# Performance work log

Hardware: AMD Instinct MI355X
Metric: run time of the kernel (lower is better)

## Reference

```python
import jax, jax.numpy as jnp
import numpy as np

SEG_LENS = (2048, 4096, 8192)
DIL_RATES = (1, 2, 4)
DIM = 1024
HEADS = 16
HEAD_DIM = DIM // HEADS
BATCH = 1
SEQ = sum(SEG_LENS)


def _hilbert_perm(L):
    """Permutation ordering the first L row-major cells of a 2^k x 2^k grid by Hilbert distance."""
    n = 1
    while n * n < L:
        n *= 2
    idx = np.arange(n * n, dtype=np.int64)
    x = idx % n
    y = idx // n
    d = np.zeros(n * n, dtype=np.int64)
    s = n // 2
    while s > 0:
        rx = ((x & s) > 0).astype(np.int64)
        ry = ((y & s) > 0).astype(np.int64)
        d += s * s * ((3 * rx) ^ ry)
        swap = ry == 0
        flip = swap & (rx == 1)
        x = np.where(flip, s - 1 - x, x)
        y = np.where(flip, s - 1 - y, y)
        x, y = np.where(swap, y, x), np.where(swap, x, y)
        s //= 2
    return np.argsort(d[:L], kind='stable')


def _segment_attn(x_seg, wqkv, bqkv, wo, bo, rate, use_hilbert=True):
    """HilbertAttentionCore: hilbert reorder -> QKV -> dilated attention -> out proj -> inverse reorder.
    x_seg: [B, L, D] -> [B, L, D]
    """
    B, L, D = x_seg.shape
    hd = D // HEADS
    perm_np = _hilbert_perm(L)
    perm = jnp.asarray(perm_np)
    inv = jnp.asarray(np.argsort(perm_np))
    xh = x_seg[:, perm] if use_hilbert else x_seg
    qkv = xh @ wqkv + bqkv                      # [B, L, 3D]
    q, k, v = jnp.split(qkv, 3, axis=-1)
    q = q.reshape(B, L, HEADS, hd)
    k = k.reshape(B, L, HEADS, hd)
    v = v.reshape(B, L, HEADS, hd)
    Lr = L // rate
    offs = jnp.arange(HEADS) % rate             # per-head dilation offset
    hidx = jnp.arange(HEADS)

    def dilate(t):
        # position i = off + rate*j  <->  reshape(L//rate, rate)[j, off]
        tr = t.reshape(B, Lr, rate, HEADS, hd)
        return tr[:, :, offs, hidx, :]          # [B, Lr, H, hd]

    qd, kd, vd = dilate(q), dilate(k), dilate(v)
    scale = 1.0 / np.sqrt(hd).astype(np.float32)
    scores = jnp.einsum('bihd,bjhd->bhij', qd, kd) * scale
    probs = jax.nn.softmax(scores, axis=-1)
    od = jnp.einsum('bhij,bjhd->bihd', probs, vd)  # [B, Lr, H, hd]
    # scatter each head's dilated subsequence back; uncovered (head,pos) stay zero
    outr = jnp.zeros((B, Lr, rate, HEADS, hd), x_seg.dtype)
    outr = outr.at[:, :, offs, hidx, :].set(od)
    out = outr.reshape(B, L, HEADS * hd) @ wo + bo
    return out[:, inv] if use_hilbert else out


def setup_inputs() -> dict:
    key = jax.random.key(0)
    ks = jax.random.split(key, 16)
    inp = {
        'q': jax.random.normal(ks[0], (BATCH, SEQ, HEADS, HEAD_DIM), jnp.float32),
        'k': jax.random.normal(ks[1], (BATCH, SEQ, HEADS, HEAD_DIM), jnp.float32),
        'v': jax.random.normal(ks[2], (BATCH, SEQ, HEADS, HEAD_DIM), jnp.float32),
    }
    for i in range(3):
        inp[f'wqkv_{i}'] = jax.random.normal(ks[3 + 4 * i], (DIM, 3 * DIM), jnp.float32) * 0.02
        inp[f'bqkv_{i}'] = jnp.zeros((3 * DIM,), jnp.float32)
        inp[f'wo_{i}'] = jax.random.normal(ks[4 + 4 * i], (DIM, DIM), jnp.float32) * 0.02
        inp[f'bo_{i}'] = jnp.zeros((DIM,), jnp.float32)
    return inp


def reference(q, k, v,
              wqkv_0, bqkv_0, wo_0, bo_0,
              wqkv_1, bqkv_1, wo_1, bo_1,
              wqkv_2, bqkv_2, wo_2, bo_2):
    B, S, H, hd = q.shape
    x = q.reshape(B, S, H * hd)  # single-GPU path uses q only (as in the source)
    params = [(wqkv_0, bqkv_0, wo_0, bo_0),
              (wqkv_1, bqkv_1, wo_1, bo_1),
              (wqkv_2, bqkv_2, wo_2, bo_2)]
    outs = []
    pos = 0
    for (seg_len, rate), (wq, bq, wo, bo) in zip(zip(SEG_LENS, DIL_RATES), params):
        if pos >= S:
            break
        end = min(pos + seg_len, S)
        outs.append(_segment_attn(x[:, pos:end], wq, bq, wo, bo, rate))
        pos = end
    return jnp.concatenate(outs, axis=1).reshape(B, S, H, hd)
```

## Files before the change

kernel.cpp:

```cpp
#include <hip/hip_runtime.h>
#include <stdint.h>
#include <stddef.h>

typedef unsigned short u16;
typedef short bf16x8 __attribute__((ext_vector_type(8)));
typedef float f32x4 __attribute__((ext_vector_type(4)));
typedef float f32x16 __attribute__((ext_vector_type(16)));
typedef unsigned short ushort8v __attribute__((ext_vector_type(8)));
typedef int i32x2 __attribute__((ext_vector_type(2)));

#define LR 2048
#define LOG2E 1.44269504088896f

__device__ __forceinline__ u16 f2bf(float f) {
  unsigned u = __float_as_uint(f);
  unsigned r = u + 0x7fffu + ((u >> 16) & 1u);
  return (u16)(r >> 16);
}

__device__ __forceinline__ unsigned cvtpk(float lo, float hi) {
  unsigned r;
  asm("v_cvt_pk_bf16_f32 %0, %1, %2" : "=v"(r) : "v"(lo), "v"(hi));
  return r;
}

__device__ __forceinline__ void plswap(unsigned& a, unsigned& b) {
#if __has_builtin(__builtin_amdgcn_permlane32_swap)
  i32x2 r = __builtin_amdgcn_permlane32_swap((int)a, (int)b, false, false);
  a = (unsigned)r[0];
  b = (unsigned)r[1];
#else
  asm volatile("s_nop 1\n\tv_permlane32_swap_b32 %0, %1\n\ts_nop 1"
               : "+v"(a), "+v"(b));
#endif
}
__device__ __forceinline__ float xhalf_sum(float x) {
  unsigned a = __float_as_uint(x), b = __float_as_uint(x);
  plswap(a, b);
  return __uint_as_float(a) + __uint_as_float(b);
}

__device__ __forceinline__ void gl_lds16(const void* g, void* l) {
  __builtin_amdgcn_global_load_lds((__attribute__((address_space(1))) void*)g,
                                   (__attribute__((address_space(3))) void*)l,
                                   16, 0, 0);
}

__device__ __forceinline__ int hilbert_perm(int idx) {
  int seg = (idx < 2048) ? 0 : (idx < 6144 ? 1 : 2);
  int segpos = (seg == 0) ? 0 : (seg == 1 ? 2048 : 6144);
  int L = 2048 << seg;
  int n = (seg == 2) ? 128 : 64;
  int t = idx - segpos;
  int d = (L == n * n) ? t : ((t < (L >> 1)) ? t : t + L);
  int x = 0, y = 0;
  for (int s = 1; s < n; s <<= 1) {
    int rx = 1 & (d >> 1);
    int ry = 1 & (d ^ rx);
    if (ry == 0) {
      if (rx == 1) { x = s - 1 - x; y = s - 1 - y; }
      int tmp = x; x = y; y = tmp;
    }
    x += s * rx; y += s * ry;
    d >>= 2;
  }
  return y * n + x;
}

__global__ void wtrans_kernel(const float* __restrict__ q0, const float* __restrict__ q1,
                              const float* __restrict__ q2, const float* __restrict__ o0,
                              const float* __restrict__ o1, const float* __restrict__ o2,
                              u16* __restrict__ dq, u16* __restrict__ dw) {
  const int seg = blockIdx.z;
  const int bx = blockIdx.x;
  const int K = 1024;
  int tx = threadIdx.x, ty = threadIdx.y;
  __shared__ float tl[32][33];
  const float* S;
  u16* D;
  int N, n0, do_remap;
  if (bx < 96) {
    S = (seg == 0) ? q0 : (seg == 1 ? q1 : q2);
    D = dq + (size_t)seg * K * 3072;
    N = 3072; n0 = bx * 32; do_remap = 0;
  } else {
    S = (seg == 0) ? o0 : (seg == 1 ? o1 : o2);
    D = dw + (size_t)seg * K * 1024;
    N = 1024; n0 = (bx - 96) * 32; do_remap = 1;
  }
  int k0 = blockIdx.y * 32;
  #pragma unroll
  for (int i = 0; i < 4; i++)
    tl[ty + 8 * i][tx] = S[(size_t)(k0 + ty + 8 * i) * N + n0 + tx];
  __syncthreads();
  int kk = k0 + tx;
  if (do_remap) {
    int rate = 1 << seg;
    int h = kk >> 6;
    int h2 = (h & (rate - 1)) * (16 >> seg) + (h >> seg);
    kk = h2 * 64 + (kk & 63);
  }
  #pragma unroll
  for (int i = 0; i < 4; i++)
    D[(size_t)(n0 + ty + 8 * i) * K + kk] = f2bf(tl[tx][ty + 8 * i]);
}

__global__ void gather_kernel(const float* __restrict__ x, u16* __restrict__ xh) {
  int rr = blockIdx.x;
  int seg = (rr < 2048) ? 0 : (rr < 6144 ? 1 : 2);
  int segpos = (seg == 0) ? 0 : (seg == 1 ? 2048 : 6144);
  int rate = 1 << seg;
  int rl = rr - segpos;
  int t = (rl & (LR - 1)) * rate + (rl >> 11);
  int orig = segpos + hilbert_perm(segpos + t);
  float4 v = *((const float4*)(x + (size_t)orig * 1024) + threadIdx.x);
  ushort4 o;
  o.x = f2bf(v.x); o.y = f2bf(v.y); o.z = f2bf(v.z); o.w = f2bf(v.w);
  *((ushort4*)(xh + (size_t)rr * 1024) + threadIdx.x) = o;
}

__global__ __launch_bounds__(512, 2) void qkv_gemm_kernel(
    const u16* __restrict__ A, const u16* __restrict__ Bt,
    const float* __restrict__ b0, const float* __restrict__ b1,
    const float* __restrict__ b2, u16* __restrict__ C) {
  __shared__ char smem[131072];
  const int tid = threadIdx.x;
  const int lane = tid & 63, wid = tid >> 6;
  const int wm = wid >> 2, wn = wid & 3;
  const int bid = blockIdx.x;
  const int xcd = bid & 7;
  const int idx = bid >> 3;
  const int grp = idx / 42;
  const int rem = idx % 42;
  const int rb = xcd * 7 + rem / 6;
  const int nb = grp * 6 + rem % 6;
  const int seg = (rb < 8) ? 0 : (rb < 24 ? 1 : 2);
  const float* bias = (seg == 0) ? b0 : (seg == 1 ? b1 : b2);
  const size_t arow0 = (size_t)rb * 256;
  const char* Ab = (const char*)(A + arow0 * 1024);
  const char* Bb = (const char*)(Bt + ((size_t)seg * 3072 + (size_t)nb * 256) * 1024);

  f32x4 acc[8][4] = {};

  #pragma unroll
  for (int it = 0; it < 4; it++) {
    int p = (it * 512 + tid) * 16;
    int e = p ^ (((p >> 7) & 7) << 4);
    int row = e >> 7, col = e & 127;
    gl_lds16(Ab + (size_t)row * 2048 + col, smem + it * 8192 + wid * 1024);
    gl_lds16(Bb + (size_t)row * 2048 + col, smem + 65536 + it * 8192 + wid * 1024);
  }
  __syncthreads();

  for (int kt = 0; kt < 16; kt++) {
    const int buf = kt & 1, nbuf = buf ^ 1;
    char* As = smem + buf * 32768;
    char* Bs = smem + 65536 + buf * 32768;
    if (kt < 15) {
      #pragma unroll
      for (int it = 0; it < 4; it++) {
        int p = (it * 512 + tid) * 16;
        int e = p ^ (((p >> 7) & 7) << 4);
        int row = e >> 7, col = e & 127;
        gl_lds16(Ab + (size_t)row * 2048 + (kt + 1) * 128 + col,
                 smem + nbuf * 32768 + it * 8192 + wid * 1024);
        gl_lds16(Bb + (size_t)row * 2048 + (kt + 1) * 128 + col,
                 smem + 65536 + nbuf * 32768 + it * 8192 + wid * 1024);
      }
    }
    #pragma unroll
    for (int kc = 0; kc < 2; kc++) {
      bf16x8 af[8], bfr[4];
      #pragma unroll
      for (int m = 0; m < 8; m++) {
        int row = wm * 128 + m * 16 + (lane & 15);
        int e = row * 128 + kc * 64 + ((lane >> 4) << 4);
        af[m] = *(const bf16x8*)(As + (e ^ ((row & 7) << 4)));
      }
      #pragma unroll
      for (int n = 0; n < 4; n++) {
        int row = wn * 64 + n * 16 + (lane & 15);
        int e = row * 128 + kc * 64 + ((lane >> 4) << 4);
        bfr[n] = *(const bf16x8*)(Bs + (e ^ ((row & 7) << 4)));
      }
      #pragma unroll
      for (int m = 0; m < 8; m++)
        #pragma unroll
        for (int n = 0; n < 4; n++)
          acc[m][n] = __builtin_amdgcn_mfma_f32_16x16x32_bf16(af[m], bfr[n], acc[m][n], 0, 0, 0);
    }
    __syncthreads();
  }

  float bv[4];
  #pragma unroll
  for (int n = 0; n < 4; n++) bv[n] = bias[nb * 256 + wn * 64 + n * 16 + (lane & 15)];
  #pragma unroll
  for (int pass = 0; pass < 2; pass++) {
    if (wm == pass) {
      #pragma unroll
      for (int m = 0; m < 8; m++)
        #pragma unroll
        for (int n = 0; n < 4; n++)
          #pragma unroll
          for (int j = 0; j < 4; j++) {
            int r = m * 16 + ((lane >> 4) << 2) + j;
            int c = wn * 64 + n * 16 + (lane & 15);
            *(u16*)(smem + r * 528 + c * 2) = f2bf(acc[m][n][j] + bv[n]);
          }
    }
    __syncthreads();
    #pragma unroll
    for (int it = 0; it < 8; it++) {
      int ci = it * 512 + tid;
      int row = ci >> 5, c16 = ci & 31;
      bf16x8 vv = *(const bf16x8*)(smem + row * 528 + c16 * 16);
      u16* crow = C + (arow0 + pass * 128 + row) * 3072 + nb * 256;
      *(bf16x8*)((char*)crow + c16 * 16) = vv;
    }
    if (pass == 0) __syncthreads();
  }
}

__global__ __launch_bounds__(256) void attn_kernel(const u16* __restrict__ qkv,
                                                   u16* __restrict__ opre) {
  __shared__ char smem[32768];
  const int tid = threadIdx.x;
  const int lane = tid & 63;
  const int wid = tid >> 6;
  const int l31 = lane & 31;
  const int hi = lane >> 5;
  const int bid = blockIdx.x;
  const int xcd = bid & 7;
  const int i = bid >> 3;
  const int by = xcd * 6 + (i >> 4);
  const int seg = by >> 4, h = by & 15;
  const int segrow = (seg == 0) ? 0 : (seg == 1 ? 2048 : 6144);
  const int rate = 1 << seg;
  const int off = h & (rate - 1);
  const int base = segrow + off * LR;
  const int h_col = off * (16 >> seg) + (h >> seg);
  const int q0 = (i & 15) * 128;
  const int qw = q0 + wid * 32;
  const char* qb = (const char*)qkv;

  const int vkey0 = 2 * (tid & 31);
  const int vd0 = (tid >> 5) * 8;

  #pragma unroll
  for (int it = 0; it < 2; it++) {
    int p = (it * 256 + tid) * 16;
    int e = p ^ (((p >> 7) & 7) << 4);
    int row = e >> 7, col = e & 127;
    gl_lds16(qb + (size_t)(base + row) * 6144 + 2048 + h * 128 + col,
             smem + it * 4096 + wid * 1024);
  }
  ushort8v v0r = *(const ushort8v*)(qb + (size_t)(base + vkey0) * 6144 + 4096 + h * 128 + vd0 * 2);
  ushort8v v1r = *(const ushort8v*)(qb + (size_t)(base + vkey0 + 1) * 6144 + 4096 + h * 128 + vd0 * 2);
  bf16x8 qf[4];
  #pragma unroll
  for (int i2 = 0; i2 < 4; i2++)
    qf[i2] = *(const bf16x8*)(qb + (size_t)(base + qw + l31) * 6144 + h * 128 + i2 * 32 + hi * 16);
  #pragma unroll
  for (int dd = 0; dd < 8; dd++) {
    int d = vd0 + dd;
    unsigned val = (unsigned)(u16)v0r[dd] | ((unsigned)(u16)v1r[dd] << 16);
    int addr = d * 128 + vkey0 * 2;
    *(unsigned*)(smem + 16384 + (addr ^ ((d & 7) << 4))) = val;
  }
  __syncthreads();

  float Lrun = 0.f;
  f32x16 accO0 = {}, accO1 = {};
  const float K1 = 0.125f * LOG2E;
  const float C2 = 4.0f * LOG2E;

  for (int kt = 0; kt < 32; kt++) {
    const int cur = kt & 1;
    const int nxt = cur ^ 1;
    char* Ks  = smem + (cur << 13);
    char* Vt  = smem + 16384 + (cur << 13);
    char* Ksn = smem + (nxt << 13);
    char* Vtn = smem + 16384 + (nxt << 13);
    ushort8v nv0, nv1;
    if (kt < 31) {
      #pragma unroll
      for (int it = 0; it < 2; it++) {
        int p = (it * 256 + tid) * 16;
        int e = p ^ (((p >> 7) & 7) << 4);
        int row = e >> 7, col = e & 127;
        gl_lds16(qb + (size_t)(base + (kt + 1) * 64 + row) * 6144 + 2048 + h * 128 + col,
                 Ksn + it * 4096 + wid * 1024);
      }
      nv0 = *(const ushort8v*)(qb + (size_t)(base + (kt + 1) * 64 + vkey0) * 6144 + 4096 + h * 128 + vd0 * 2);
      nv1 = *(const ushort8v*)(qb + (size_t)(base + (kt + 1) * 64 + vkey0 + 1) * 6144 + 4096 + h * 128 + vd0 * 2);
    }
    #pragma unroll
    for (int s = 0; s < 2; s++) {
      f32x16 sacc = {};
      __builtin_amdgcn_s_setprio(1);
      #pragma unroll
      for (int i2 = 0; i2 < 4; i2++) {
        int row = s * 32 + l31;
        int addr = (row * 128 + i2 * 32 + hi * 16) ^ ((row & 7) << 4);
        bf16x8 kf = *(const bf16x8*)(Ks + addr);
        sacc = __builtin_amdgcn_mfma_f32_32x32x16_bf16(kf, qf[i2], sacc, 0, 0, 0);
      }
      __builtin_amdgcn_s_setprio(0);
      #pragma unroll
      for (int r = 0; r < 16; r++) sacc[r] = exp2f(sacc[r] * K1 - C2);
      float s8[8];
      #pragma unroll
      for (int t = 0; t < 8; t++) s8[t] = sacc[2 * t] + sacc[2 * t + 1];
      float sm = (((s8[0] + s8[1]) + (s8[2] + s8[3])) + ((s8[4] + s8[5]) + (s8[6] + s8[7])));
      Lrun += xhalf_sum(sm);
      unsigned w[8];
      #pragma unroll
      for (int t = 0; t < 8; t++) w[t] = cvtpk(sacc[2 * t], sacc[2 * t + 1]);
      plswap(w[0], w[2]); plswap(w[1], w[3]);
      plswap(w[4], w[6]); plswap(w[5], w[7]);
      union PU { unsigned u[4]; bf16x8 v; };
      PU pu0, pu1;
      pu0.u[0] = w[0]; pu0.u[1] = w[1]; pu0.u[2] = w[2]; pu0.u[3] = w[3];
      pu1.u[0] = w[4]; pu1.u[1] = w[5]; pu1.u[2] = w[6]; pu1.u[3] = w[7];
      __builtin_amdgcn_s_setprio(1);
      #pragma unroll
      for (int j = 0; j < 2; j++) {
        bf16x8 pa = (j == 0) ? pu0.v : pu1.v;
        #pragma unroll
        for (int dt = 0; dt < 2; dt++) {
          int d = dt * 32 + l31;
          int addr = (d * 128 + s * 64 + j * 32 + hi * 16) ^ ((d & 7) << 4);
          bf16x8 vf = *(const bf16x8*)(Vt + addr);
          if (dt == 0) accO0 = __builtin_amdgcn_mfma_f32_32x32x16_bf16(pa, vf, accO0, 0, 0, 0);
          else         accO1 = __builtin_amdgcn_mfma_f32_32x32x16_bf16(pa, vf, accO1, 0, 0, 0);
        }
      }
      __builtin_amdgcn_s_setprio(0);
    }
    if (kt < 31) {
      #pragma unroll
      for (int dd = 0; dd < 8; dd++) {
        int d = vd0 + dd;
        unsigned val = (unsigned)(u16)nv0[dd] | ((unsigned)(u16)nv1[dd] << 16);
        int addr = d * 128 + vkey0 * 2;
        *(unsigned*)(Vtn + (addr ^ ((d & 7) << 4))) = val;
      }
    }
    __syncthreads();
  }

  float invL = 1.0f / Lrun;
  #pragma unroll
  for (int r = 0; r < 16; r++) {
    int qrow = (r & 3) + 8 * (r >> 2) + 4 * hi;
    float li = __shfl(invL, qrow);
    int qloc = wid * 32 + qrow;
    int a0 = (qloc * 128 + l31 * 2) ^ ((qrow & 7) << 4);
    int a1 = (qloc * 128 + 64 + l31 * 2) ^ ((qrow & 7) << 4);
    *(u16*)(smem + a0) = f2bf(accO0[r] * li);
    *(u16*)(smem + a1) = f2bf(accO1[r] * li);
  }
  __syncthreads();
  #pragma unroll
  for (int it = 0; it < 4; it++) {
    int idx = it * 256 + tid;
    int row = idx >> 3, c16 = idx & 7;
    int a = (row * 128 + c16 * 16) ^ ((row & 7) << 4);
    bf16x8 vv = *(const bf16x8*)(smem + a);
    *(bf16x8*)((char*)(opre + (size_t)(base + q0 + row) * 1024 + h_col * 64) + c16 * 16) = vv;
  }
}

__global__ __launch_bounds__(256) void out_gemm_kernel(
    const u16* __restrict__ A, const u16* __restrict__ Bt,
    const float* __restrict__ b0, const float* __restrict__ b1,
    const float* __restrict__ b2, float* __restrict__ Out) {
  __shared__ char smem[65536];
  __shared__ int drow[128];
  const int tid = threadIdx.x;
  const int lane = tid & 63, wid = tid >> 6;
  const int wm = wid >> 1, wn = wid & 1;
  const int rb = blockIdx.x, nb = blockIdx.y;
  const int seg = (rb < 16) ? 0 : (rb < 48 ? 1 : 2);
  const int segpos = (seg == 0) ? 0 : (seg == 1 ? 2048 : 6144);
  const int rate = 1 << seg;
  const float* bias = (seg == 0) ? b0 : (seg == 1 ? b1 : b2);
  const size_t arow0 = (size_t)rb * 128;
  const char* Ab = (const char*)(A + arow0 * 1024);
  const char* Bb = (const char*)(Bt + ((size_t)seg * 1024 + (size_t)nb * 128) * 1024);

  const int blk = (int)(arow0 - segpos) >> 11;
  const int ktpb = 16 >> seg;
  const int kt0 = blk * ktpb;

  f32x4 acc[4][4] = {};

  if (tid < 128) {
    int rl = (int)arow0 + tid - segpos;
    int t = (rl & (LR - 1)) * rate + (rl >> 11);
    drow[tid] = segpos + hilbert_perm(segpos + t);
  }

  #pragma unroll
  for (int it = 0; it < 4; it++) {
    int p = (it * 256 + tid) * 16;
    int e = p ^ (((p >> 7) & 7) << 4);
    int row = e >> 7, col = e & 127;
    gl_lds16(Ab + (size_t)row * 2048 + kt0 * 128 + col, smem + it * 4096 + wid * 1024);
    gl_lds16(Bb + (size_t)row * 2048 + kt0 * 128 + col, smem + 32768 + it * 4096 + wid * 1024);
  }
  __syncthreads();

  for (int i = 0; i < ktpb; i++) {
    const int kt = kt0 + i;
    const int buf = i & 1, nbuf = buf ^ 1;
    char* As = smem + buf * 16384;
    char* Bs = smem + 32768 + buf * 16384;
    if (i < ktpb - 1) {
      #pragma unroll
      for (int it = 0; it < 4; it++) {
        int p = (it * 256 + tid) * 16;
        int e = p ^ (((p >> 7) & 7) << 4);
        int row = e >> 7, col = e & 127;
        gl_lds16(Ab + (size_t)row * 2048 + (kt + 1) * 128 + col,
                 smem + nbuf * 16384 + it * 4096 + wid * 1024);
        gl_lds16(Bb + (size_t)row * 2048 + (kt + 1) * 128 + col,
                 smem + 32768 + nbuf * 16384 + it * 4096 + wid * 1024);
      }
    }
    #pragma unroll
    for (int kc = 0; kc < 2; kc++) {
      bf16x8 af[4], bfr[4];
      #pragma unroll
      for (int m = 0; m < 4; m++) {
        int row = wm * 64 + m * 16 + (lane & 15);
        int e = row * 128 + kc * 64 + ((lane >> 4) << 4);
        af[m] = *(const bf16x8*)(As + (e ^ ((row & 7) << 4)));
      }
      #pragma unroll
      for (int n = 0; n < 4; n++) {
        int row = wn * 64 + n * 16 + (lane & 15);
        int e = row * 128 + kc * 64 + ((lane >> 4) << 4);
        bfr[n] = *(const bf16x8*)(Bs + (e ^ ((row & 7) << 4)));
      }
      #pragma unroll
      for (int m = 0; m < 4; m++)
        #pragma unroll
        for (int n = 0; n < 4; n++)
          acc[m][n] = __builtin_amdgcn_mfma_f32_16x16x32_bf16(af[m], bfr[n], acc[m][n], 0, 0, 0);
    }
    __syncthreads();
  }
  float bv[4];
  #pragma unroll
  for (int n = 0; n < 4; n++) bv[n] = bias[nb * 128 + wn * 64 + n * 16 + (lane & 15)];
  #pragma unroll
  for (int m = 0; m < 4; m++)
    #pragma unroll
    for (int j = 0; j < 4; j++) {
      int r = wm * 64 + m * 16 + ((lane >> 4) << 2) + j;
      int gr = drow[r];
      float* orow = Out + (size_t)gr * 1024 + nb * 128 + wn * 64;
      #pragma unroll
      for (int n = 0; n < 4; n++)
        orow[n * 16 + (lane & 15)] = acc[m][n][j] + bv[n];
    }
}

extern "C" void kernel_launch(void* const* d_in, const int* in_sizes, int n_in,
                              void* d_out, int out_size, void* d_ws, size_t ws_size,
                              hipStream_t stream) {
  (void)in_sizes; (void)n_in; (void)out_size;
  const float* x = (const float*)d_in[0];
  const float* wqkv0 = (const float*)d_in[3];
  const float* bqkv0 = (const float*)d_in[4];
  const float* wo0 = (const float*)d_in[5];
  const float* bo0 = (const float*)d_in[6];
  const float* wqkv1 = (const float*)d_in[7];
  const float* bqkv1 = (const float*)d_in[8];
  const float* wo1 = (const float*)d_in[9];
  const float* bo1 = (const float*)d_in[10];
  const float* wqkv2 = (const float*)d_in[11];
  const float* bqkv2 = (const float*)d_in[12];
  const float* wo2 = (const float*)d_in[13];
  const float* bo2 = (const float*)d_in[14];

  if (ws_size < 172032000ull) return;
  char* ws = (char*)d_ws;
  u16* xh    = (u16*)(ws + 65536);
  u16* wqkvt = (u16*)(ws + 29425664);
  u16* wot   = (u16*)(ws + 48300032);
  u16* qkv   = (u16*)(ws + 54591488);
  u16* opre  = (u16*)(ws + 142671872);
  float* out = (float*)d_out;

  wtrans_kernel<<<dim3(128, 32, 3), dim3(32, 8), 0, stream>>>(wqkv0, wqkv1, wqkv2,
                                                              wo0, wo1, wo2, wqkvt, wot);
  gather_kernel<<<14336, 256, 0, stream>>>(x, xh);
  qkv_gemm_kernel<<<672, 512, 0, stream>>>(xh, wqkvt, bqkv0, bqkv1, bqkv2, qkv);
  attn_kernel<<<768, 256, 0, stream>>>(qkv, opre);
  out_gemm_kernel<<<dim3(112, 8), 256, 0, stream>>>(opre, wot, bo0, bo1, bo2, out);
}
```

Measured before the change: 273.7 us.

## Double attention query tile to 256 rows with 512-thread blocks

The attention kernel now processes 256 query rows per block with 8 waves instead of 128 rows with 4 waves. Each K/V tile staged in shared memory is therefore reused by twice as many queries, which halves global K/V traffic per query. The grid becomes a 2D (8, 48) launch, dropping the previous XCD-aware block remapping. With only 384 blocks across the CUs, work may be unevenly spread and L2 locality may suffer; only half the threads perform the V transpose staging.

```diff
diff --git a/kernel.cpp b/kernel.cpp
--- a/kernel.cpp
+++ b/kernel.cpp
@@ -222,51 +222,53 @@
   }
 }
 
-__global__ __launch_bounds__(256) void attn_kernel(const u16* __restrict__ qkv,
-                                                   u16* __restrict__ opre) {
+__global__ __launch_bounds__(512, 4) void attn_kernel(const u16* __restrict__ qkv,
+                                                      u16* __restrict__ opre) {
   __shared__ char smem[32768];
   const int tid = threadIdx.x;
   const int lane = tid & 63;
   const int wid = tid >> 6;
   const int l31 = lane & 31;
   const int hi = lane >> 5;
-  const int bid = blockIdx.x;
-  const int xcd = bid & 7;
-  const int i = bid >> 3;
-  const int by = xcd * 6 + (i >> 4);
+  const int by = blockIdx.y;
   const int seg = by >> 4, h = by & 15;
   const int segrow = (seg == 0) ? 0 : (seg == 1 ? 2048 : 6144);
   const int rate = 1 << seg;
   const int off = h & (rate - 1);
   const int base = segrow + off * LR;
   const int h_col = off * (16 >> seg) + (h >> seg);
-  const int q0 = (i & 15) * 128;
+  const int q0 = blockIdx.x * 256;
   const int qw = q0 + wid * 32;
   const char* qb = (const char*)qkv;
 
+  const bool vact = (tid < 256);
   const int vkey0 = 2 * (tid & 31);
-  const int vd0 = (tid >> 5) * 8;
-
-  #pragma unroll
-  for (int it = 0; it < 2; it++) {
-    int p = (it * 256 + tid) * 16;
+  const int vd0 = ((tid & 255) >> 5) * 8;
+
+  {
+    int p = tid * 16;
     int e = p ^ (((p >> 7) & 7) << 4);
     int row = e >> 7, col = e & 127;
     gl_lds16(qb + (size_t)(base + row) * 6144 + 2048 + h * 128 + col,
-             smem + it * 4096 + wid * 1024);
-  }
-  ushort8v v0r = *(const ushort8v*)(qb + (size_t)(base + vkey0) * 6144 + 4096 + h * 128 + vd0 * 2);
-  ushort8v v1r = *(const ushort8v*)(qb + (size_t)(base + vkey0 + 1) * 6144 + 4096 + h * 128 + vd0 * 2);
+             smem + wid * 1024);
+  }
+  ushort8v v0r = {}, v1r = {};
+  if (vact) {
+    v0r = *(const ushort8v*)(qb + (size_t)(base + vkey0) * 6144 + 4096 + h * 128 + vd0 * 2);
+    v1r = *(const ushort8v*)(qb + (size_t)(base + vkey0 + 1) * 6144 + 4096 + h * 128 + vd0 * 2);
+  }
   bf16x8 qf[4];
   #pragma unroll
   for (int i2 = 0; i2 < 4; i2++)
     qf[i2] = *(const bf16x8*)(qb + (size_t)(base + qw + l31) * 6144 + h * 128 + i2 * 32 + hi * 16);
-  #pragma unroll
-  for (int dd = 0; dd < 8; dd++) {
-    int d = vd0 + dd;
-    unsigned val = (unsigned)(u16)v0r[dd] | ((unsigned)(u16)v1r[dd] << 16);
-    int addr = d * 128 + vkey0 * 2;
-    *(unsigned*)(smem + 16384 + (addr ^ ((d & 7) << 4))) = val;
+  if (vact) {
+    #pragma unroll
+    for (int dd = 0; dd < 8; dd++) {
+      int d = vd0 + dd;
+      unsigned val = (unsigned)(u16)v0r[dd] | ((unsigned)(u16)v1r[dd] << 16);
+      int addr = d * 128 + vkey0 * 2;
+      *(unsigned*)(smem + 16384 + (addr ^ ((d & 7) << 4))) = val;
+    }
   }
   __syncthreads();
 
@@ -282,18 +284,19 @@
     char* Vt  = smem + 16384 + (cur << 13);
     char* Ksn = smem + (nxt << 13);
     char* Vtn = smem + 16384 + (nxt << 13);
-    ushort8v nv0, nv1;
+    ushort8v nv0 = {}, nv1 = {};
     if (kt < 31) {
-      #pragma unroll
-      for (int it = 0; it < 2; it++) {
-        int p = (it * 256 + tid) * 16;
+      {
+        int p = tid * 16;
         int e = p ^ (((p >> 7) & 7) << 4);
         int row = e >> 7, col = e & 127;
         gl_lds16(qb + (size_t)(base + (kt + 1) * 64 + row) * 6144 + 2048 + h * 128 + col,
-                 Ksn + it * 4096 + wid * 1024);
-      }
-      nv0 = *(const ushort8v*)(qb + (size_t)(base + (kt + 1) * 64 + vkey0) * 6144 + 4096 + h * 128 + vd0 * 2);
-      nv1 = *(const ushort8v*)(qb + (size_t)(base + (kt + 1) * 64 + vkey0 + 1) * 6144 + 4096 + h * 128 + vd0 * 2);
+                 Ksn + wid * 1024);
+      }
+      if (vact) {
+        nv0 = *(const ushort8v*)(qb + (size_t)(base + (kt + 1) * 64 + vkey0) * 6144 + 4096 + h * 128 + vd0 * 2);
+        nv1 = *(const ushort8v*)(qb + (size_t)(base + (kt + 1) * 64 + vkey0 + 1) * 6144 + 4096 + h * 128 + vd0 * 2);
+      }
     }
     #pragma unroll
     for (int s = 0; s < 2; s++) {
@@ -338,7 +341,7 @@
       }
       __builtin_amdgcn_s_setprio(0);
     }
-    if (kt < 31) {
+    if (kt < 31 && vact) {
       #pragma unroll
       for (int dd = 0; dd < 8; dd++) {
         int d = vd0 + dd;
@@ -364,7 +367,7 @@
   __syncthreads();
   #pragma unroll
   for (int it = 0; it < 4; it++) {
-    int idx = it * 256 + tid;
+    int idx = it * 512 + tid;
     int row = idx >> 3, c16 = idx & 7;
     int a = (row * 128 + c16 * 16) ^ ((row & 7) << 4);
     bf16x8 vv = *(const bf16x8*)(smem + a);
@@ -499,6 +502,6 @@
                                                               wo0, wo1, wo2, wqkvt, wot);
   gather_kernel<<<14336, 256, 0, stream>>>(x, xh);
   qkv_gemm_kernel<<<672, 512, 0, stream>>>(xh, wqkvt, bqkv0, bqkv1, bqkv2, qkv);
-  attn_kernel<<<768, 256, 0, stream>>>(qkv, opre);
+  attn_kernel<<<dim3(8, 48), 512, 0, stream>>>(qkv, opre);
   out_gemm_kernel<<<dim3(112, 8), 256, 0, stream>>>(opre, wot, bo0, bo1, bo2, out);
 }
```

New measurement: 281.2 us. 1.03x slower.

## Fuse weight transpose and gather into one prep kernel; simplify attn grid mapping

Applied to the files above, without the earlier changes.

Merges the weight transpose/convert kernel and the Hilbert gather kernel into a single launch that dispatches on block index, removing one kernel launch and the idle gap between them. Separately, the attention kernel drops its XCD-aware block swizzle in favour of a plain 2D grid (query tile, segment-head). That gives up the intended L2 locality per XCD, where blocks of the same head share K/V, in exchange for simpler indexing.

```diff
diff --git a/kernel.cpp b/kernel.cpp
--- a/kernel.cpp
+++ b/kernel.cpp
@@ -67,56 +67,61 @@
   return y * n + x;
 }
 
-__global__ void wtrans_kernel(const float* __restrict__ q0, const float* __restrict__ q1,
-                              const float* __restrict__ q2, const float* __restrict__ o0,
-                              const float* __restrict__ o1, const float* __restrict__ o2,
-                              u16* __restrict__ dq, u16* __restrict__ dw) {
-  const int seg = blockIdx.z;
-  const int bx = blockIdx.x;
-  const int K = 1024;
-  int tx = threadIdx.x, ty = threadIdx.y;
+__global__ void prep_kernel(const float* __restrict__ q0, const float* __restrict__ q1,
+                            const float* __restrict__ q2, const float* __restrict__ o0,
+                            const float* __restrict__ o1, const float* __restrict__ o2,
+                            const float* __restrict__ x,
+                            u16* __restrict__ dq, u16* __restrict__ dw,
+                            u16* __restrict__ xh) {
   __shared__ float tl[32][33];
-  const float* S;
-  u16* D;
-  int N, n0, do_remap;
-  if (bx < 96) {
-    S = (seg == 0) ? q0 : (seg == 1 ? q1 : q2);
-    D = dq + (size_t)seg * K * 3072;
-    N = 3072; n0 = bx * 32; do_remap = 0;
+  const int b = blockIdx.x;
+  const int tid = threadIdx.x;
+  if (b < 12288) {
+    const int bx = b & 127;
+    const int ky = (b >> 7) & 31;
+    const int seg = b >> 12;
+    const int K = 1024;
+    const int tx = tid & 31, ty = tid >> 5;
+    const float* S;
+    u16* D;
+    int N, n0, do_remap;
+    if (bx < 96) {
+      S = (seg == 0) ? q0 : (seg == 1 ? q1 : q2);
+      D = dq + (size_t)seg * K * 3072;
+      N = 3072; n0 = bx * 32; do_remap = 0;
+    } else {
+      S = (seg == 0) ? o0 : (seg == 1 ? o1 : o2);
+      D = dw + (size_t)seg * K * 1024;
+      N = 1024; n0 = (bx - 96) * 32; do_remap = 1;
+    }
+    int k0 = ky * 32;
+    #pragma unroll
+    for (int i = 0; i < 4; i++)
+      tl[ty + 8 * i][tx] = S[(size_t)(k0 + ty + 8 * i) * N + n0 + tx];
+    __syncthreads();
+    int kk = k0 + tx;
+    if (do_remap) {
+      int rate = 1 << seg;
+      int h = kk >> 6;
+      int h2 = (h & (rate - 1)) * (16 >> seg) + (h >> seg);
+      kk = h2 * 64 + (kk & 63);
+    }
+    #pragma unroll
+    for (int i = 0; i < 4; i++)
+      D[(size_t)(n0 + ty + 8 * i) * K + kk] = f2bf(tl[tx][ty + 8 * i]);
   } else {
-    S = (seg == 0) ? o0 : (seg == 1 ? o1 : o2);
-    D = dw + (size_t)seg * K * 1024;
-    N = 1024; n0 = (bx - 96) * 32; do_remap = 1;
-  }
-  int k0 = blockIdx.y * 32;
-  #pragma unroll
-  for (int i = 0; i < 4; i++)
-    tl[ty + 8 * i][tx] = S[(size_t)(k0 + ty + 8 * i) * N + n0 + tx];
-  __syncthreads();
-  int kk = k0 + tx;
-  if (do_remap) {
+    int rr = b - 12288;
+    int seg = (rr < 2048) ? 0 : (rr < 6144 ? 1 : 2);
+    int segpos = (seg == 0) ? 0 : (seg == 1 ? 2048 : 6144);
     int rate = 1 << seg;
-    int h = kk >> 6;
-    int h2 = (h & (rate - 1)) * (16 >> seg) + (h >> seg);
-    kk = h2 * 64 + (kk & 63);
-  }
-  #pragma unroll
-  for (int i = 0; i < 4; i++)
-    D[(size_t)(n0 + ty + 8 * i) * K + kk] = f2bf(tl[tx][ty + 8 * i]);
-}
-
-__global__ void gather_kernel(const float* __restrict__ x, u16* __restrict__ xh) {
-  int rr = blockIdx.x;
-  int seg = (rr < 2048) ? 0 : (rr < 6144 ? 1 : 2);
-  int segpos = (seg == 0) ? 0 : (seg == 1 ? 2048 : 6144);
-  int rate = 1 << seg;
-  int rl = rr - segpos;
-  int t = (rl & (LR - 1)) * rate + (rl >> 11);
-  int orig = segpos + hilbert_perm(segpos + t);
-  float4 v = *((const float4*)(x + (size_t)orig * 1024) + threadIdx.x);
-  ushort4 o;
-  o.x = f2bf(v.x); o.y = f2bf(v.y); o.z = f2bf(v.z); o.w = f2bf(v.w);
-  *((ushort4*)(xh + (size_t)rr * 1024) + threadIdx.x) = o;
+    int rl = rr - segpos;
+    int t = (rl & (LR - 1)) * rate + (rl >> 11);
+    int orig = segpos + hilbert_perm(segpos + t);
+    float4 v = *((const float4*)(x + (size_t)orig * 1024) + tid);
+    ushort4 o;
+    o.x = f2bf(v.x); o.y = f2bf(v.y); o.z = f2bf(v.z); o.w = f2bf(v.w);
+    *((ushort4*)(xh + (size_t)rr * 1024) + tid) = o;
+  }
 }
 
 __global__ __launch_bounds__(512, 2) void qkv_gemm_kernel(
@@ -230,17 +235,14 @@
   const int wid = tid >> 6;
   const int l31 = lane & 31;
   const int hi = lane >> 5;
-  const int bid = blockIdx.x;
-  const int xcd = bid & 7;
-  const int i = bid >> 3;
-  const int by = xcd * 6 + (i >> 4);
+  const int by = blockIdx.y;
   const int seg = by >> 4, h = by & 15;
   const int segrow = (seg == 0) ? 0 : (seg == 1 ? 2048 : 6144);
   const int rate = 1 << seg;
   const int off = h & (rate - 1);
   const int base = segrow + off * LR;
   const int h_col = off * (16 >> seg) + (h >> seg);
-  const int q0 = (i & 15) * 128;
+  const int q0 = blockIdx.x * 128;
   const int qw = q0 + wid * 32;
   const char* qb = (const char*)qkv;
 
@@ -495,10 +497,9 @@
   u16* opre  = (u16*)(ws + 142671872);
   float* out = (float*)d_out;
 
-  wtrans_kernel<<<dim3(128, 32, 3), dim3(32, 8), 0, stream>>>(wqkv0, wqkv1, wqkv2,
-                                                              wo0, wo1, wo2, wqkvt, wot);
-  gather_kernel<<<14336, 256, 0, stream>>>(x, xh);
+  prep_kernel<<<26624, 256, 0, stream>>>(wqkv0, wqkv1, wqkv2, wo0, wo1, wo2,
+                                         x, wqkvt, wot, xh);
   qkv_gemm_kernel<<<672, 512, 0, stream>>>(xh, wqkvt, bqkv0, bqkv1, bqkv2, qkv);
-  attn_kernel<<<768, 256, 0, stream>>>(qkv, opre);
+  attn_kernel<<<dim3(16, 48), 256, 0, stream>>>(qkv, opre);
   out_gemm_kernel<<<dim3(112, 8), 256, 0, stream>>>(opre, wot, bo0, bo1, bo2, out);
 }
```

Measured after the change: 270.7 us. No clear change (-1.1%).
